# Optimization experiments

Measured on AMD Instinct MI355X. Metric: run time of the kernel, lower is better.

## Reference

```python
import jax, jax.numpy as jnp
import numpy as np

N_SRC, N_DST, N_EDGE, D_IN, D_HID, D_OUT = 100000, 25000, 300000, 256, 256, 256


def setup_inputs() -> dict:
    key = jax.random.key(0)
    ks = jax.random.split(key, 9)
    # forward tensor args
    h_src = jax.random.normal(ks[0], (N_SRC, D_IN), dtype=jnp.float32)
    h_dst = jax.random.normal(ks[1], (N_DST, D_IN), dtype=jnp.float32)
    weights = jax.random.uniform(ks[2], (N_EDGE,), dtype=jnp.float32)
    src_idx = jax.random.randint(ks[3], (N_EDGE,), 0, N_SRC)
    dst_idx = jax.random.randint(ks[4], (N_EDGE,), 0, N_DST)
    # learned parameters (xavier_uniform with relu gain, zero bias)
    gain = float(np.sqrt(2.0))
    def xavier(k, fan_in, fan_out):
        a = gain * np.sqrt(6.0 / (fan_in + fan_out))
        return jax.random.uniform(k, (fan_in, fan_out), dtype=jnp.float32, minval=-a, maxval=a)
    Q_w = xavier(ks[5], D_IN, D_HID)            # stored [in, out]
    Q_b = jnp.zeros((D_HID,), dtype=jnp.float32)
    W_w = xavier(ks[6], D_IN + D_HID, D_OUT)    # stored [in, out]
    W_b = jnp.zeros((D_OUT,), dtype=jnp.float32)
    return {"h_src": h_src, "h_dst": h_dst, "weights": weights,
            "Q_w": Q_w, "Q_b": Q_b, "W_w": W_w, "W_b": W_b,
            "src_idx": src_idx, "dst_idx": dst_idx}


def reference(h_src, h_dst, weights, Q_w, Q_b, W_w, W_b, src_idx, dst_idx):
    n_dst = h_dst.shape[0]
    # nft = relu(Q(h_src))  (dropout is eval-mode identity)
    nft = jax.nn.relu(h_src @ Q_w + Q_b)                     # [N_src, H]
    # weighted neighbor sum: u_mul_e + sum over edges per dst node
    msg = nft[src_idx] * weights[:, None]                    # [E, H]
    n = jax.ops.segment_sum(msg, dst_idx, num_segments=n_dst)          # [N_dst, H]
    ws = jax.ops.segment_sum(weights, dst_idx, num_segments=n_dst)     # [N_dst]
    ws = jnp.clip(ws, 1.0, None)[:, None]
    z = jax.nn.relu(jnp.concatenate([n / ws, h_dst], axis=1) @ W_w + W_b)  # [N_dst, O]
    z_norm = jnp.linalg.norm(z, ord=2, axis=1, keepdims=True)
    z_norm = jnp.where(z_norm == 0, jnp.float32(1.0), z_norm)
    return z / z_norm
```

## Files before the change

### kernel.cpp

```cpp
#include <hip/hip_runtime.h>
#include <hip/hip_bf16.h>
#include <cstdint>

#define N_SRC 100000
#define N_DST 25000
#define N_EDGE 300000

typedef float f32x4 __attribute__((ext_vector_type(4)));
typedef __bf16 bf16x8 __attribute__((ext_vector_type(8)));

__device__ __forceinline__ unsigned short f2bf(float f) {
    union { float f; unsigned int u; } v; v.f = f;
    unsigned int u = v.u;
    u += 0x7FFFu + ((u >> 16) & 1u);
    return (unsigned short)(u >> 16);
}
__device__ __forceinline__ float bf2f(unsigned int bits16) {
    union { unsigned int u; float f; } v; v.u = bits16 << 16;
    return v.f;
}

__global__ void cast_weights(const float* __restrict__ Qw, const float* __restrict__ Ww,
                             unsigned short* __restrict__ Qt, unsigned short* __restrict__ Wt) {
    int i = blockIdx.x * blockDim.x + threadIdx.x;
    if (i < 256 * 256) {
        int n = i >> 8, k = i & 255;
        Qt[n * 256 + k] = f2bf(Qw[k * 256 + n]);
    } else if (i < 256 * 256 + 512 * 256) {
        int j = i - 256 * 256;
        int n = j >> 9, k = j & 511;
        Wt[n * 512 + k] = f2bf(Ww[k * 256 + n]);
    }
}

__global__ void hist_kernel(const int* __restrict__ dst_idx, int* __restrict__ counts) {
    int i = blockIdx.x * blockDim.x + threadIdx.x;
    if (i < N_EDGE) atomicAdd(&counts[dst_idx[i]], 1);
}

__global__ __launch_bounds__(1024) void scan_kernel(const int* __restrict__ counts,
                                                    int* __restrict__ offsets, int n) {
    __shared__ int wsum[16];
    const int t = threadIdx.x;
    const int wid = t >> 6, lane = t & 63;
    int carry = 0;
    if (t == 0) offsets[0] = 0;
    for (int base = 0; base < n; base += 1024) {
        int x = (base + t < n) ? counts[base + t] : 0;
        #pragma unroll
        for (int off = 1; off < 64; off <<= 1) {
            int y = __shfl_up(x, off, 64);
            if (lane >= off) x += y;
        }
        if (lane == 63) wsum[wid] = x;
        __syncthreads();
        if (t < 16) {
            int w = wsum[t];
            #pragma unroll
            for (int off = 1; off < 16; off <<= 1) {
                int y = __shfl_up(w, off, 64);
                if (t >= off) w += y;
            }
            wsum[t] = w;
        }
        __syncthreads();
        int pre = (wid > 0) ? wsum[wid - 1] : 0;
        int incl = carry + pre + x;
        if (base + t < n) offsets[base + t + 1] = incl;
        carry += wsum[15];
        __syncthreads();
    }
}

__global__ void scatter_kernel(const int* __restrict__ dst_idx, const int* __restrict__ offsets,
                               int* __restrict__ counts, int* __restrict__ edge_list) {
    int i = blockIdx.x * blockDim.x + threadIdx.x;
    if (i < N_EDGE) {
        int d = dst_idx[i];
        int pos = offsets[d] + (atomicSub(&counts[d], 1) - 1);
        edge_list[pos] = i;
    }
}

template<int KDIM, bool A_BF16, bool NORM>
__global__ __launch_bounds__(256, 2) void gemm_fused(
    const float* __restrict__ Af, const unsigned short* __restrict__ Ab,
    const unsigned short* __restrict__ Bt, const float* __restrict__ bias,
    unsigned short* __restrict__ Cb, float* __restrict__ Cf, int M)
{
    constexpr int NKT = KDIM / 64;
    __shared__ __align__(16) unsigned short As[2][64 * 72];
    __shared__ float norml[4][64];

    const int tid = threadIdx.x;
    const int wave = tid >> 6, lane = tid & 63;
    const int g = lane >> 4, c = lane & 15;
    const int wn0 = wave * 64;
    const int m0 = blockIdx.x * 64;

    f32x4 acc[4][4];
    #pragma unroll
    for (int i = 0; i < 4; ++i)
        #pragma unroll
        for (int j = 0; j < 4; ++j)
            acc[i][j] = (f32x4){0.f, 0.f, 0.f, 0.f};

    float4 sf[4];
    uint4  sb[2];

    auto issueA = [&](int kt) {
        const int k0 = kt * 64;
        if constexpr (A_BF16) {
            #pragma unroll
            for (int i = 0; i < 2; ++i) {
                int idx = tid + i * 256;
                int row = idx >> 3, ch = idx & 7;
                int gm = min(m0 + row, M - 1);
                sb[i] = *reinterpret_cast<const uint4*>(Ab + (size_t)gm * KDIM + k0 + ch * 8);
            }
        } else {
            #pragma unroll
            for (int i = 0; i < 4; ++i) {
                int idx = tid + i * 256;
                int row = idx >> 4, c4 = idx & 15;
                int gm = min(m0 + row, M - 1);
                sf[i] = *reinterpret_cast<const float4*>(Af + (size_t)gm * KDIM + k0 + c4 * 4);
            }
        }
    };
    auto writeA = [&](int buf) {
        if constexpr (A_BF16) {
            #pragma unroll
            for (int i = 0; i < 2; ++i) {
                int idx = tid + i * 256;
                int row = idx >> 3, ch = idx & 7;
                *reinterpret_cast<uint4*>(&As[buf][row * 72 + ch * 8]) = sb[i];
            }
        } else {
            #pragma unroll
            for (int i = 0; i < 4; ++i) {
                int idx = tid + i * 256;
                int row = idx >> 4, c4 = idx & 15;
                uint2 p;
                p.x = (unsigned)f2bf(sf[i].x) | ((unsigned)f2bf(sf[i].y) << 16);
                p.y = (unsigned)f2bf(sf[i].z) | ((unsigned)f2bf(sf[i].w) << 16);
                *reinterpret_cast<uint2*>(&As[buf][row * 72 + c4 * 4]) = p;
            }
        }
    };

    issueA(0);
    writeA(0);
    __syncthreads();

    #pragma unroll
    for (int kt = 0; kt < NKT; ++kt) {
        const int cur = kt & 1;
        if (kt + 1 < NKT) issueA(kt + 1);
        const int k0 = kt * 64;
        bf16x8 bfrag[2][4];
        #pragma unroll
        for (int ks = 0; ks < 2; ++ks)
            #pragma unroll
            for (int ni = 0; ni < 4; ++ni)
                bfrag[ks][ni] = *reinterpret_cast<const bf16x8*>(
                    Bt + (size_t)(wn0 + ni * 16 + c) * KDIM + k0 + ks * 32 + g * 8);
        #pragma unroll
        for (int ks = 0; ks < 2; ++ks) {
            const int koff = ks * 32 + g * 8;
            bf16x8 a[4];
            #pragma unroll
            for (int mi = 0; mi < 4; ++mi)
                a[mi] = *reinterpret_cast<const bf16x8*>(&As[cur][(mi * 16 + c) * 72 + koff]);
            #pragma unroll
            for (int mi = 0; mi < 4; ++mi)
                #pragma unroll
                for (int ni = 0; ni < 4; ++ni)
                    acc[mi][ni] = __builtin_amdgcn_mfma_f32_16x16x32_bf16(a[mi], bfrag[ks][ni], acc[mi][ni], 0, 0, 0);
        }
        if (kt + 1 < NKT) writeA(cur ^ 1);
        __syncthreads();
    }

    float bcol[4];
    #pragma unroll
    for (int ni = 0; ni < 4; ++ni) bcol[ni] = bias[wn0 + ni * 16 + c];

    if constexpr (!NORM) {
        #pragma unroll
        for (int mi = 0; mi < 4; ++mi) {
            int rowb = m0 + mi * 16 + g * 4;
            #pragma unroll
            for (int ni = 0; ni < 4; ++ni) {
                int col = wn0 + ni * 16 + c;
                #pragma unroll
                for (int r = 0; r < 4; ++r) {
                    int row = rowb + r;
                    if (row < M) {
                        float v = fmaxf(acc[mi][ni][r] + bcol[ni], 0.f);
                        Cb[(size_t)row * 256 + col] = f2bf(v);
                    }
                }
            }
        }
    } else {
        float ssq[4][4];
        #pragma unroll
        for (int mi = 0; mi < 4; ++mi) {
            #pragma unroll
            for (int r = 0; r < 4; ++r) {
                float s = 0.f;
                #pragma unroll
                for (int ni = 0; ni < 4; ++ni) {
                    float v = fmaxf(acc[mi][ni][r] + bcol[ni], 0.f);
                    acc[mi][ni][r] = v;
                    s += v * v;
                }
                #pragma unroll
                for (int m = 1; m < 16; m <<= 1) s += __shfl_xor(s, m, 64);
                ssq[mi][r] = s;
            }
        }
        if (c == 0) {
            #pragma unroll
            for (int mi = 0; mi < 4; ++mi)
                #pragma unroll
                for (int r = 0; r < 4; ++r)
                    norml[wave][mi * 16 + g * 4 + r] = ssq[mi][r];
        }
        __syncthreads();
        #pragma unroll
        for (int mi = 0; mi < 4; ++mi) {
            int rowb = m0 + mi * 16 + g * 4;
            #pragma unroll
            for (int r = 0; r < 4; ++r) {
                int rl = mi * 16 + g * 4 + r;
                float tot = norml[0][rl] + norml[1][rl] + norml[2][rl] + norml[3][rl];
                float rn = tot > 0.f ? rsqrtf(tot) : 1.0f;
                int row = rowb + r;
                if (row < M) {
                    #pragma unroll
                    for (int ni = 0; ni < 4; ++ni) {
                        int col = wn0 + ni * 16 + c;
                        Cf[(size_t)row * 256 + col] = acc[mi][ni][r] * rn;
                    }
                }
            }
        }
    }
}

__global__ __launch_bounds__(256) void aggregate_kernel(
    const unsigned short* __restrict__ nft, const float* __restrict__ h_dst,
    const float* __restrict__ weights, const int* __restrict__ src_idx,
    const int* __restrict__ edge_list, const int* __restrict__ offsets,
    unsigned short* __restrict__ xb)
{
    int d = blockIdx.x * 4 + (threadIdx.x >> 6);
    if (d >= N_DST) return;
    int lane = threadIdx.x & 63;
    int p0 = offsets[d], p1 = offsets[d + 1];
    float a0 = 0.f, a1 = 0.f, a2 = 0.f, a3 = 0.f, wsum = 0.f;
    int p = p0;
    for (; p + 1 < p1; p += 2) {
        int e0 = edge_list[p], e1 = edge_list[p + 1];
        float w0 = weights[e0], w1 = weights[e1];
        int s0 = src_idx[e0], s1 = src_idx[e1];
        uint2 v0 = *reinterpret_cast<const uint2*>(nft + (size_t)s0 * 256 + lane * 4);
        uint2 v1 = *reinterpret_cast<const uint2*>(nft + (size_t)s1 * 256 + lane * 4);
        wsum += w0 + w1;
        a0 += w0 * bf2f(v0.x & 0xffffu) + w1 * bf2f(v1.x & 0xffffu);
        a1 += w0 * bf2f(v0.x >> 16)     + w1 * bf2f(v1.x >> 16);
        a2 += w0 * bf2f(v0.y & 0xffffu) + w1 * bf2f(v1.y & 0xffffu);
        a3 += w0 * bf2f(v0.y >> 16)     + w1 * bf2f(v1.y >> 16);
    }
    if (p < p1) {
        int e = edge_list[p];
        float w = weights[e];
        int s = src_idx[e];
        wsum += w;
        uint2 v = *reinterpret_cast<const uint2*>(nft + (size_t)s * 256 + lane * 4);
        a0 += w * bf2f(v.x & 0xffffu);
        a1 += w * bf2f(v.x >> 16);
        a2 += w * bf2f(v.y & 0xffffu);
        a3 += w * bf2f(v.y >> 16);
    }
    float inv = 1.0f / fmaxf(wsum, 1.0f);
    uint2 pk;
    pk.x = (unsigned)f2bf(a0 * inv) | ((unsigned)f2bf(a1 * inv) << 16);
    pk.y = (unsigned)f2bf(a2 * inv) | ((unsigned)f2bf(a3 * inv) << 16);
    *reinterpret_cast<uint2*>(xb + (size_t)d * 512 + lane * 4) = pk;
    float4 h = *reinterpret_cast<const float4*>(h_dst + (size_t)d * 256 + lane * 4);
    uint2 q;
    q.x = (unsigned)f2bf(h.x) | ((unsigned)f2bf(h.y) << 16);
    q.y = (unsigned)f2bf(h.z) | ((unsigned)f2bf(h.w) << 16);
    *reinterpret_cast<uint2*>(xb + (size_t)d * 512 + 256 + lane * 4) = q;
}

extern "C" void kernel_launch(void* const* d_in, const int* in_sizes, int n_in,
                              void* d_out, int out_size, void* d_ws, size_t ws_size,
                              hipStream_t stream) {
    const float* h_src   = (const float*)d_in[0];
    const float* h_dst   = (const float*)d_in[1];
    const float* weights = (const float*)d_in[2];
    const float* Q_w     = (const float*)d_in[3];
    const float* Q_b     = (const float*)d_in[4];
    const float* W_w     = (const float*)d_in[5];
    const float* W_b     = (const float*)d_in[6];
    const int* src_idx   = (const int*)d_in[7];
    const int* dst_idx   = (const int*)d_in[8];
    float* out = (float*)d_out;

    char* ws = (char*)d_ws;
    unsigned short* nft = (unsigned short*)(ws);
    unsigned short* xb  = (unsigned short*)(ws + 51200000);
    unsigned short* Qt  = (unsigned short*)(ws + 76800000);
    unsigned short* Wt  = (unsigned short*)(ws + 76931072);
    int* counts    = (int*)(ws + 77193216);
    int* offsets   = (int*)(ws + 77293216);
    int* edge_list = (int*)(ws + 77393220);

    hipMemsetAsync(counts, 0, N_DST * sizeof(int), stream);

    cast_weights<<<768, 256, 0, stream>>>(Q_w, W_w, Qt, Wt);
    hist_kernel<<<(N_EDGE + 255) / 256, 256, 0, stream>>>(dst_idx, counts);
    scan_kernel<<<1, 1024, 0, stream>>>(counts, offsets, N_DST);
    scatter_kernel<<<(N_EDGE + 255) / 256, 256, 0, stream>>>(dst_idx, offsets, counts, edge_list);

    gemm_fused<256, false, false><<<(N_SRC + 63) / 64, 256, 0, stream>>>(
        h_src, nullptr, Qt, Q_b, nft, nullptr, N_SRC);

    aggregate_kernel<<<N_DST / 4, 256, 0, stream>>>(
        nft, h_dst, weights, src_idx, edge_list, offsets, xb);

    gemm_fused<512, true, true><<<(N_DST + 63) / 64, 256, 0, stream>>>(
        nullptr, xb, Wt, W_b, nullptr, out, N_DST);

    (void)in_sizes; (void)n_in; (void)out_size; (void)ws_size;
}
```

Measured before the change: 188.8 us.

## Stage GEMM A tiles via direct global-to-LDS loads with XOR swizzle

Splits the templated GEMM into two specialized kernels that load A tiles straight into shared memory with global_load_lds instead of going through registers. The first GEMM now keeps fp32 tiles in LDS and converts to bf16 at fragment-read time, and both use an XOR swizzle in place of padding to avoid bank conflicts. The intent is to cut register-staging overhead and let the next tile's loads overlap the MFMA work. The cost is twice the LDS per tile for the fp32 path, extra conversion work in the inner loop, and dropping the occupancy hint in launch_bounds.

```diff
diff --git a/kernel.cpp b/kernel.cpp
--- a/kernel.cpp
+++ b/kernel.cpp
@@ -8,6 +8,9 @@
 
 typedef float f32x4 __attribute__((ext_vector_type(4)));
 typedef __bf16 bf16x8 __attribute__((ext_vector_type(8)));
+
+typedef const __attribute__((address_space(1))) void gv_t;
+typedef __attribute__((address_space(3))) void lv_t;
 
 __device__ __forceinline__ unsigned short f2bf(float f) {
     union { float f; unsigned int u; } v; v.f = f;
@@ -82,21 +85,16 @@
     }
 }
 
-template<int KDIM, bool A_BF16, bool NORM>
-__global__ __launch_bounds__(256, 2) void gemm_fused(
-    const float* __restrict__ Af, const unsigned short* __restrict__ Ab,
-    const unsigned short* __restrict__ Bt, const float* __restrict__ bias,
-    unsigned short* __restrict__ Cb, float* __restrict__ Cf, int M)
+__global__ __launch_bounds__(256) void gemm1_97(
+    const float* __restrict__ Af, const unsigned short* __restrict__ Bt,
+    const float* __restrict__ bias, unsigned short* __restrict__ Cb)
 {
-    constexpr int NKT = KDIM / 64;
-    __shared__ __align__(16) unsigned short As[2][64 * 72];
-    __shared__ float norml[4][64];
-
+    __shared__ __align__(16) float Asf[2][64 * 64];
     const int tid = threadIdx.x;
-    const int wave = tid >> 6, lane = tid & 63;
-    const int g = lane >> 4, c = lane & 15;
-    const int wn0 = wave * 64;
+    const int wv = tid >> 6, lane = tid & 63, g = lane >> 4, cl = lane & 15;
     const int m0 = blockIdx.x * 64;
+    const int n0 = wv * 64;
+    const int srow = tid >> 4, sblk = tid & 15;
 
     f32x4 acc[4][4];
     #pragma unroll
@@ -105,146 +103,172 @@
         for (int j = 0; j < 4; ++j)
             acc[i][j] = (f32x4){0.f, 0.f, 0.f, 0.f};
 
-    float4 sf[4];
-    uint4  sb[2];
-
-    auto issueA = [&](int kt) {
-        const int k0 = kt * 64;
-        if constexpr (A_BF16) {
-            #pragma unroll
-            for (int i = 0; i < 2; ++i) {
-                int idx = tid + i * 256;
-                int row = idx >> 3, ch = idx & 7;
-                int gm = min(m0 + row, M - 1);
-                sb[i] = *reinterpret_cast<const uint4*>(Ab + (size_t)gm * KDIM + k0 + ch * 8);
-            }
-        } else {
-            #pragma unroll
-            for (int i = 0; i < 4; ++i) {
-                int idx = tid + i * 256;
-                int row = idx >> 4, c4 = idx & 15;
-                int gm = min(m0 + row, M - 1);
-                sf[i] = *reinterpret_cast<const float4*>(Af + (size_t)gm * KDIM + k0 + c4 * 4);
-            }
+    auto stage = [&](int buf, int kt) {
+        #pragma unroll
+        for (int i = 0; i < 4; ++i) {
+            const int row = i * 16 + srow;
+            const int grow = min(m0 + row, N_SRC - 1);
+            const float* gp = Af + (size_t)grow * 256 + kt * 64 + ((sblk ^ (row & 7)) << 2);
+            __builtin_amdgcn_global_load_lds(
+                (gv_t*)gp,
+                (lv_t*)((char*)&Asf[buf][0] + i * 4096 + wv * 1024), 16, 0, 0);
         }
     };
-    auto writeA = [&](int buf) {
-        if constexpr (A_BF16) {
-            #pragma unroll
-            for (int i = 0; i < 2; ++i) {
-                int idx = tid + i * 256;
-                int row = idx >> 3, ch = idx & 7;
-                *reinterpret_cast<uint4*>(&As[buf][row * 72 + ch * 8]) = sb[i];
-            }
-        } else {
-            #pragma unroll
-            for (int i = 0; i < 4; ++i) {
-                int idx = tid + i * 256;
-                int row = idx >> 4, c4 = idx & 15;
-                uint2 p;
-                p.x = (unsigned)f2bf(sf[i].x) | ((unsigned)f2bf(sf[i].y) << 16);
-                p.y = (unsigned)f2bf(sf[i].z) | ((unsigned)f2bf(sf[i].w) << 16);
-                *reinterpret_cast<uint2*>(&As[buf][row * 72 + c4 * 4]) = p;
-            }
-        }
-    };
-
-    issueA(0);
-    writeA(0);
+
+    stage(0, 0);
     __syncthreads();
 
     #pragma unroll
-    for (int kt = 0; kt < NKT; ++kt) {
-        const int cur = kt & 1;
-        if (kt + 1 < NKT) issueA(kt + 1);
-        const int k0 = kt * 64;
-        bf16x8 bfrag[2][4];
+    for (int kt = 0; kt < 4; ++kt) {
+        const int buf = kt & 1;
+        if (kt < 3) stage(buf ^ 1, kt + 1);
+
+        uint4 bfrag[2][4];
         #pragma unroll
         for (int ks = 0; ks < 2; ++ks)
             #pragma unroll
             for (int ni = 0; ni < 4; ++ni)
-                bfrag[ks][ni] = *reinterpret_cast<const bf16x8*>(
-                    Bt + (size_t)(wn0 + ni * 16 + c) * KDIM + k0 + ks * 32 + g * 8);
+                bfrag[ks][ni] = *reinterpret_cast<const uint4*>(
+                    Bt + (size_t)(n0 + ni * 16 + cl) * 256 + kt * 64 + ks * 32 + g * 8);
+
         #pragma unroll
         for (int ks = 0; ks < 2; ++ks) {
-            const int koff = ks * 32 + g * 8;
-            bf16x8 a[4];
-            #pragma unroll
-            for (int mi = 0; mi < 4; ++mi)
-                a[mi] = *reinterpret_cast<const bf16x8*>(&As[cur][(mi * 16 + c) * 72 + koff]);
-            #pragma unroll
-            for (int mi = 0; mi < 4; ++mi)
+            #pragma unroll
+            for (int mi = 0; mi < 4; ++mi) {
+                const int row = mi * 16 + cl;
+                const f32x4 lo = *reinterpret_cast<const f32x4*>(
+                    (const char*)&Asf[buf][0] + row * 256 + (((ks * 8 + g * 2 + 0) ^ (cl & 7)) << 4));
+                const f32x4 hi = *reinterpret_cast<const f32x4*>(
+                    (const char*)&Asf[buf][0] + row * 256 + (((ks * 8 + g * 2 + 1) ^ (cl & 7)) << 4));
+                bf16x8 af;
+                af[0] = (__bf16)lo[0]; af[1] = (__bf16)lo[1]; af[2] = (__bf16)lo[2]; af[3] = (__bf16)lo[3];
+                af[4] = (__bf16)hi[0]; af[5] = (__bf16)hi[1]; af[6] = (__bf16)hi[2]; af[7] = (__bf16)hi[3];
                 #pragma unroll
                 for (int ni = 0; ni < 4; ++ni)
-                    acc[mi][ni] = __builtin_amdgcn_mfma_f32_16x16x32_bf16(a[mi], bfrag[ks][ni], acc[mi][ni], 0, 0, 0);
-        }
-        if (kt + 1 < NKT) writeA(cur ^ 1);
+                    acc[mi][ni] = __builtin_amdgcn_mfma_f32_16x16x32_bf16(
+                        af, __builtin_bit_cast(bf16x8, bfrag[ks][ni]), acc[mi][ni], 0, 0, 0);
+            }
+        }
         __syncthreads();
     }
 
     float bcol[4];
     #pragma unroll
-    for (int ni = 0; ni < 4; ++ni) bcol[ni] = bias[wn0 + ni * 16 + c];
-
-    if constexpr (!NORM) {
-        #pragma unroll
-        for (int mi = 0; mi < 4; ++mi) {
-            int rowb = m0 + mi * 16 + g * 4;
+    for (int ni = 0; ni < 4; ++ni) bcol[ni] = bias[n0 + ni * 16 + cl];
+    #pragma unroll
+    for (int mi = 0; mi < 4; ++mi) {
+        const int rowb = m0 + mi * 16 + g * 4;
+        #pragma unroll
+        for (int ni = 0; ni < 4; ++ni) {
+            const int col = n0 + ni * 16 + cl;
+            #pragma unroll
+            for (int r = 0; r < 4; ++r) {
+                const int row = rowb + r;
+                if (row < N_SRC) {
+                    float v = fmaxf(acc[mi][ni][r] + bcol[ni], 0.f);
+                    Cb[(size_t)row * 256 + col] = f2bf(v);
+                }
+            }
+        }
+    }
+}
+
+__global__ __launch_bounds__(256) void gemm2_97(
+    const unsigned short* __restrict__ Ab, const unsigned short* __restrict__ Bt,
+    const float* __restrict__ bias, float* __restrict__ Cf, int M)
+{
+    __shared__ __align__(16) unsigned short Ash[2][64 * 64];
+    __shared__ float norml[4][64];
+    const int tid = threadIdx.x;
+    const int wv = tid >> 6, lane = tid & 63, g = lane >> 4, cl = lane & 15;
+    const int m0 = blockIdx.x * 64;
+    const int n0 = wv * 64;
+    const int srow = tid >> 3, sblk = tid & 7;
+
+    f32x4 acc[4][4];
+    #pragma unroll
+    for (int i = 0; i < 4; ++i)
+        #pragma unroll
+        for (int j = 0; j < 4; ++j)
+            acc[i][j] = (f32x4){0.f, 0.f, 0.f, 0.f};
+
+    auto stage = [&](int buf, int kt) {
+        #pragma unroll
+        for (int i = 0; i < 2; ++i) {
+            const int row = i * 32 + srow;
+            const int grow = min(m0 + row, M - 1);
+            const unsigned short* gp = Ab + (size_t)grow * 512 + kt * 64 + ((sblk ^ (row & 7)) << 3);
+            __builtin_amdgcn_global_load_lds(
+                (gv_t*)gp,
+                (lv_t*)((char*)&Ash[buf][0] + i * 4096 + wv * 1024), 16, 0, 0);
+        }
+    };
+
+    stage(0, 0);
+    __syncthreads();
+
+    #pragma unroll
+    for (int kt = 0; kt < 8; ++kt) {
+        const int buf = kt & 1;
+        if (kt < 7) stage(buf ^ 1, kt + 1);
+
+        uint4 bfrag[2][4];
+        #pragma unroll
+        for (int ks = 0; ks < 2; ++ks)
+            #pragma unroll
+            for (int ni = 0; ni < 4; ++ni)
+                bfrag[ks][ni] = *reinterpret_cast<const uint4*>(
+                    Bt + (size_t)(n0 + ni * 16 + cl) * 512 + kt * 64 + ks * 32 + g * 8);
+
+        #pragma unroll
+        for (int ks = 0; ks < 2; ++ks) {
+            #pragma unroll
+            for (int mi = 0; mi < 4; ++mi) {
+                const int row = mi * 16 + cl;
+                const bf16x8 af = *reinterpret_cast<const bf16x8*>(
+                    (const char*)&Ash[buf][0] + row * 128 + (((ks * 4 + g) ^ (cl & 7)) << 4));
+                #pragma unroll
+                for (int ni = 0; ni < 4; ++ni)
+                    acc[mi][ni] = __builtin_amdgcn_mfma_f32_16x16x32_bf16(
+                        af, __builtin_bit_cast(bf16x8, bfrag[ks][ni]), acc[mi][ni], 0, 0, 0);
+            }
+        }
+        __syncthreads();
+    }
+
+    float bcol[4];
+    #pragma unroll
+    for (int ni = 0; ni < 4; ++ni) bcol[ni] = bias[n0 + ni * 16 + cl];
+
+    #pragma unroll
+    for (int mi = 0; mi < 4; ++mi) {
+        #pragma unroll
+        for (int r = 0; r < 4; ++r) {
+            float s = 0.f;
             #pragma unroll
             for (int ni = 0; ni < 4; ++ni) {
-                int col = wn0 + ni * 16 + c;
+                float v = fmaxf(acc[mi][ni][r] + bcol[ni], 0.f);
+                acc[mi][ni][r] = v;
+                s += v * v;
+            }
+            #pragma unroll
+            for (int m = 1; m < 16; m <<= 1) s += __shfl_xor(s, m, 64);
+            if (cl == 0) norml[wv][mi * 16 + g * 4 + r] = s;
+        }
+    }
+    __syncthreads();
+    #pragma unroll
+    for (int mi = 0; mi < 4; ++mi) {
+        #pragma unroll
+        for (int r = 0; r < 4; ++r) {
+            const int rl = mi * 16 + g * 4 + r;
+            const float tot = norml[0][rl] + norml[1][rl] + norml[2][rl] + norml[3][rl];
+            const float rn = tot > 0.f ? rsqrtf(tot) : 1.0f;
+            const int row = m0 + rl;
+            if (row < M) {
                 #pragma unroll
-                for (int r = 0; r < 4; ++r) {
-                    int row = rowb + r;
-                    if (row < M) {
-                        float v = fmaxf(acc[mi][ni][r] + bcol[ni], 0.f);
-                        Cb[(size_t)row * 256 + col] = f2bf(v);
-                    }
-                }
-            }
-        }
-    } else {
-        float ssq[4][4];
-        #pragma unroll
-        for (int mi = 0; mi < 4; ++mi) {
-            #pragma unroll
-            for (int r = 0; r < 4; ++r) {
-                float s = 0.f;
-                #pragma unroll
-                for (int ni = 0; ni < 4; ++ni) {
-                    float v = fmaxf(acc[mi][ni][r] + bcol[ni], 0.f);
-                    acc[mi][ni][r] = v;
-                    s += v * v;
-                }
-                #pragma unroll
-                for (int m = 1; m < 16; m <<= 1) s += __shfl_xor(s, m, 64);
-                ssq[mi][r] = s;
-            }
-        }
-        if (c == 0) {
-            #pragma unroll
-            for (int mi = 0; mi < 4; ++mi)
-                #pragma unroll
-                for (int r = 0; r < 4; ++r)
-                    norml[wave][mi * 16 + g * 4 + r] = ssq[mi][r];
-        }
-        __syncthreads();
-        #pragma unroll
-        for (int mi = 0; mi < 4; ++mi) {
-            int rowb = m0 + mi * 16 + g * 4;
-            #pragma unroll
-            for (int r = 0; r < 4; ++r) {
-                int rl = mi * 16 + g * 4 + r;
-                float tot = norml[0][rl] + norml[1][rl] + norml[2][rl] + norml[3][rl];
-                float rn = tot > 0.f ? rsqrtf(tot) : 1.0f;
-                int row = rowb + r;
-                if (row < M) {
-                    #pragma unroll
-                    for (int ni = 0; ni < 4; ++ni) {
-                        int col = wn0 + ni * 16 + c;
-                        Cf[(size_t)row * 256 + col] = acc[mi][ni][r] * rn;
-                    }
-                }
+                for (int ni = 0; ni < 4; ++ni)
+                    Cf[(size_t)row * 256 + n0 + ni * 16 + cl] = acc[mi][ni][r] * rn;
             }
         }
     }
@@ -327,14 +351,12 @@
     scan_kernel<<<1, 1024, 0, stream>>>(counts, offsets, N_DST);
     scatter_kernel<<<(N_EDGE + 255) / 256, 256, 0, stream>>>(dst_idx, offsets, counts, edge_list);
 
-    gemm_fused<256, false, false><<<(N_SRC + 63) / 64, 256, 0, stream>>>(
-        h_src, nullptr, Qt, Q_b, nft, nullptr, N_SRC);
+    gemm1_97<<<(N_SRC + 63) / 64, 256, 0, stream>>>(h_src, Qt, Q_b, nft);
 
     aggregate_kernel<<<N_DST / 4, 256, 0, stream>>>(
         nft, h_dst, weights, src_idx, edge_list, offsets, xb);
 
-    gemm_fused<512, true, true><<<(N_DST + 63) / 64, 256, 0, stream>>>(
-        nullptr, xb, Wt, W_b, nullptr, out, N_DST);
+    gemm2_97<<<(N_DST + 63) / 64, 256, 0, stream>>>(xb, Wt, W_b, out, N_DST);
 
     (void)in_sizes; (void)n_in; (void)out_size; (void)ws_size;
 }
```

Result: no change. 191.2 us (+1.3%).
